# Kernel optimization log

Hardware: AMD Instinct MI355X
Metric: run time of the kernel (lower is better)

The kernel has to match this reference:

```python
import jax, jax.numpy as jnp
import numpy as np

B, S, E, H = 4, 2048, 1024, 64

def setup_inputs() -> dict:
    key = jax.random.key(0)
    k1, k2, k3, k4 = jax.random.split(key, 4)
    return {
        "x": jax.random.normal(k1, (B, S, E), dtype=jnp.float32),
        "Wq": jax.random.normal(k2, (E, H), dtype=jnp.float32) * (E ** -0.5),
        "Wk": jax.random.normal(k3, (E, H), dtype=jnp.float32) * (E ** -0.5),
        "Wv": jax.random.normal(k4, (E, H), dtype=jnp.float32) * (E ** -0.5),
    }

def reference(x, Wq, Wk, Wv):
    b, s, e = x.shape
    q = jnp.einsum('bse,eh->bsh', x, Wq)   # [B,S,H]
    k = jnp.einsum('bse,eh->bsh', x, Wk)
    v = jnp.einsum('bse,eh->bsh', x, Wv)
    # NOTE: source scales by sqrt(embedding_dimension), not sqrt(head_dim)
    scores = jnp.einsum('bqh,bkh->bqk', q, k) / (e ** 0.5)  # [B,S,S]
    causal = jnp.tril(jnp.ones((s, s), dtype=bool))
    scores = jnp.where(causal, scores, -jnp.inf)
    attn = jax.nn.softmax(scores.astype(jnp.float32), axis=-1)
    return jnp.einsum('bqk,bkh->bqh', attn, v)  # [B,S,H]
```

## Files before the change

### kernel.cpp

```cpp
#include <hip/hip_runtime.h>
#include <hip/hip_bf16.h>
#include <math.h>

#define BB 4
#define SS 2048
#define EE 1024
#define HH 64
#define BS (BB*SS)

typedef __attribute__((ext_vector_type(8))) short bf16x8;
typedef __attribute__((ext_vector_type(4))) float f32x4;

static __device__ __forceinline__ unsigned int f2b(float f) {
  __hip_bfloat16 h = __float2bfloat16(f);
  unsigned short u;
  __builtin_memcpy(&u, &h, 2);
  return (unsigned int)u;
}

__global__ __launch_bounds__(256) void wt_prep(const float* __restrict__ Wq,
                                               const float* __restrict__ Wk,
                                               const float* __restrict__ Wv,
                                               unsigned short* __restrict__ wt) {
  __shared__ float tile[64 * 69];
  const int blk = blockIdx.x;
  const int w = blk >> 4;
  const int et = blk & 15;
  const int t = threadIdx.x;
  const float* __restrict__ W = (w == 0) ? Wq : ((w == 1) ? Wk : Wv);

#pragma unroll
  for (int i = 0; i < 4; ++i) {
    const int idx = t + i * 256;
    const int row = idx >> 4;
    const int f4 = idx & 15;
    const float4 v = *(const float4*)(W + ((size_t)(et * 64 + row)) * 64 + f4 * 4);
    tile[row * 69 + f4 * 4 + 0] = v.x;
    tile[row * 69 + f4 * 4 + 1] = v.y;
    tile[row * 69 + f4 * 4 + 2] = v.z;
    tile[row * 69 + f4 * 4 + 3] = v.w;
  }
  __syncthreads();

  const float scale = (w == 0) ? 0.03125f * 1.4426950408889634f : 1.0f;
  const int h = t >> 2;
  const int eg = (t & 3) * 16;
  unsigned int o[8];
#pragma unroll
  for (int i = 0; i < 8; ++i) {
    const float a = tile[(eg + 2 * i + 0) * 69 + h] * scale;
    const float b = tile[(eg + 2 * i + 1) * 69 + h] * scale;
    o[i] = f2b(a) | (f2b(b) << 16);
  }
  unsigned short* dst = wt + ((size_t)(w * 64 + h)) * 1024 + et * 64 + eg;
  uint4 lo4; lo4.x = o[0]; lo4.y = o[1]; lo4.z = o[2]; lo4.w = o[3];
  uint4 hi4; hi4.x = o[4]; hi4.y = o[5]; hi4.z = o[6]; hi4.w = o[7];
  *(uint4*)dst = lo4;
  *(uint4*)(dst + 8) = hi4;
}

__global__ __launch_bounds__(512) void qkv_mfma(const float* __restrict__ x,
                                                const unsigned short* __restrict__ wt,
                                                unsigned short* __restrict__ qb,
                                                unsigned short* __restrict__ kbuf,
                                                unsigned short* __restrict__ vtb) {
  __shared__ char smem[57344];
  const int t = threadIdx.x;
  const int blk = blockIdx.x;
  const int lane = t & 63;
  const int wv = t >> 6;
  const int wm = wv >> 2;
  const int wn = wv & 3;
  const int lo = lane & 15, hi = lane >> 4;

  const int xrow = t >> 4;
  const int xf4 = t & 15;
  const int wr0 = t >> 3;
  const int wc = t & 7;

  const float* __restrict__ xsrc = x + ((size_t)blk * 32 + xrow) * 1024 + xf4 * 4;
  const unsigned short* __restrict__ wsrc = wt + (size_t)wr0 * 1024 + wc * 8;

  float4 xr;
  bf16x8 wrg[3];

  f32x4 acc[3] = {};

#define LOADT(kt)                                                     \
  do {                                                                \
    xr = *(const float4*)(xsrc + (kt) * 64);                          \
    wrg[0] = *(const bf16x8*)(wsrc + (kt) * 64);                      \
    wrg[1] = *(const bf16x8*)(wsrc + 64 * 1024 + (kt) * 64);          \
    wrg[2] = *(const bf16x8*)(wsrc + 128 * 1024 + (kt) * 64);         \
  } while (0)

#define WRITET(buf)                                                          \
  do {                                                                       \
    uint2 pv;                                                                \
    pv.x = f2b(xr.x) | (f2b(xr.y) << 16);                                    \
    pv.y = f2b(xr.z) | (f2b(xr.w) << 16);                                    \
    *(uint2*)&smem[(buf) * 4096 + xrow * 128 +                               \
                   ((xf4 * 8) ^ ((xrow & 7) << 4))] = pv;                    \
    char* wb = &smem[8192 + (buf) * 24576];                                  \
    const int sw = (wc * 16) ^ ((wr0 & 7) << 4);                             \
    *(bf16x8*)&wb[(wr0 + 0) * 128 + sw] = wrg[0];                            \
    *(bf16x8*)&wb[(wr0 + 64) * 128 + sw] = wrg[1];                           \
    *(bf16x8*)&wb[(wr0 + 128) * 128 + sw] = wrg[2];                          \
  } while (0)

  LOADT(0);
  WRITET(0);
  __syncthreads();

  const int arow = wm * 16 + lo;
  const int aswz = (arow & 7) << 4;

  for (int kt = 0; kt < 16; ++kt) {
    const int cur = kt & 1;
    if (kt < 15) LOADT(kt + 1);

    const char* xb = &smem[cur * 4096];
    const char* wb = &smem[8192 + cur * 24576];
    const bf16x8 a0 = *(const bf16x8*)&xb[arow * 128 + ((hi * 16) ^ aswz)];
    const bf16x8 a1 = *(const bf16x8*)&xb[arow * 128 + ((64 + hi * 16) ^ aswz)];
#pragma unroll
    for (int nf = 0; nf < 3; ++nf) {
      const int brow = wn * 48 + nf * 16 + lo;
      const int bswz = (brow & 7) << 4;
      const bf16x8 b0 = *(const bf16x8*)&wb[brow * 128 + ((hi * 16) ^ bswz)];
      const bf16x8 b1 = *(const bf16x8*)&wb[brow * 128 + ((64 + hi * 16) ^ bswz)];
      acc[nf] = __builtin_amdgcn_mfma_f32_16x16x32_bf16(a0, b0, acc[nf], 0, 0, 0);
      acc[nf] = __builtin_amdgcn_mfma_f32_16x16x32_bf16(a1, b1, acc[nf], 0, 0, 0);
    }

    if (kt < 15) WRITET(cur ^ 1);
    __syncthreads();
  }

  const int m0 = blk * 32 + wm * 16 + hi * 4;
#pragma unroll
  for (int nf = 0; nf < 3; ++nf) {
    const int nb = wn * 48 + nf * 16;
    const int which = nb >> 6;
    const int h = (nb & 63) + lo;
#pragma unroll
    for (int r = 0; r < 4; ++r) {
      const int row = m0 + r;
      const unsigned short v = (unsigned short)f2b(acc[nf][r]);
      if (which == 0) qb[(size_t)row * 64 + h] = v;
      else if (which == 1) kbuf[(size_t)row * 64 + h] = v;
      else vtb[((size_t)(row >> 11) * 64 + h) * 2048 + (row & 2047)] = v;
    }
  }
#undef LOADT
#undef WRITET
}

__global__ __launch_bounds__(512) void attn_mfma(const unsigned short* __restrict__ qb,
                                                 const unsigned short* __restrict__ kbuf,
                                                 const unsigned short* __restrict__ vt,
                                                 float* __restrict__ out) {
  __shared__ __align__(16) float sacc[8][16][64];
  __shared__ float sml[2][8][16];

  const int t = threadIdx.x;
  const int lane = t & 63;
  const int w = t >> 6;
  const int lo = lane & 15, hi = lane >> 4;
  const int hi4 = hi * 4;

  const int blk = blockIdx.x;
  const int batch = blk & 3;
  const int tt = blk >> 2;
  const int qt = (tt & 1) ? (63 - (tt >> 1)) : (tt >> 1);
  const int q0 = qt * 32;

  const unsigned short* Qb = qb   + (size_t)batch * SS * 64;
  const unsigned short* Kb = kbuf + (size_t)batch * SS * 64;
  const unsigned short* Vt = vt   + (size_t)batch * 64 * SS;

  const int qA = q0 + lo;
  const int qBr = q0 + 16 + lo;

  const bf16x8 qf0a = *(const bf16x8*)(Qb + (size_t)qA * 64 + hi * 8);
  const bf16x8 qf1a = *(const bf16x8*)(Qb + (size_t)qA * 64 + 32 + hi * 8);
  const bf16x8 qf0b = *(const bf16x8*)(Qb + (size_t)qBr * 64 + hi * 8);
  const bf16x8 qf1b = *(const bf16x8*)(Qb + (size_t)qBr * 64 + 32 + hi * 8);

  f32x4 accA[4] = {}, accB[4] = {};
  float mA = -1e30f, lA = 0.f, mB = -1e30f, lB = 0.f;

  const int kend = q0 + 32;
  for (int kbase = w * 64; kbase < kend; kbase += 512) {
    f32x4 sA[4], sB[4];
    __builtin_amdgcn_s_setprio(1);
#pragma unroll
    for (int j0 = 0; j0 < 4; ++j0) {
      const unsigned short* Krow = Kb + (size_t)(kbase + j0 * 16 + lo) * 64 + hi * 8;
      const bf16x8 ka = *(const bf16x8*)(Krow);
      const bf16x8 kb2 = *(const bf16x8*)(Krow + 32);
      f32x4 ca = {}, cb = {};
      ca = __builtin_amdgcn_mfma_f32_16x16x32_bf16(ka, qf0a, ca, 0, 0, 0);
      ca = __builtin_amdgcn_mfma_f32_16x16x32_bf16(kb2, qf1a, ca, 0, 0, 0);
      cb = __builtin_amdgcn_mfma_f32_16x16x32_bf16(ka, qf0b, cb, 0, 0, 0);
      cb = __builtin_amdgcn_mfma_f32_16x16x32_bf16(kb2, qf1b, cb, 0, 0, 0);
      sA[j0] = ca; sB[j0] = cb;
    }
    __builtin_amdgcn_s_setprio(0);

    bf16x8 va[2][4];
#pragma unroll
    for (int kc = 0; kc < 2; ++kc)
#pragma unroll
      for (int j = 0; j < 4; ++j)
        va[kc][j] = *(const bf16x8*)(Vt + (size_t)(j * 16 + lo) * SS +
                                     kbase + kc * 32 + hi * 8);

    if (kbase + 64 > q0) {
#pragma unroll
      for (int j0 = 0; j0 < 4; ++j0)
#pragma unroll
        for (int r = 0; r < 4; ++r) {
          const int key = kbase + j0 * 16 + hi4 + r;
          sA[j0][r] = (key > qA) ? -1e30f : sA[j0][r];
          sB[j0][r] = (key > qBr) ? -1e30f : sB[j0][r];
        }
    }

    unsigned int WA[4][2], WB[4][2];
    {
      float mx = fmaxf(fmaxf(sA[0][0], sA[0][1]), fmaxf(sA[0][2], sA[0][3]));
      mx = fmaxf(mx, fmaxf(fmaxf(sA[1][0], sA[1][1]), fmaxf(sA[1][2], sA[1][3])));
      mx = fmaxf(mx, fmaxf(fmaxf(sA[2][0], sA[2][1]), fmaxf(sA[2][2], sA[2][3])));
      mx = fmaxf(mx, fmaxf(fmaxf(sA[3][0], sA[3][1]), fmaxf(sA[3][2], sA[3][3])));
      mx = fmaxf(mx, __shfl_xor(mx, 16));
      mx = fmaxf(mx, __shfl_xor(mx, 32));
      if (__any(mx > mA)) {
        const float mnew = fmaxf(mA, mx);
        const float sc = exp2f(mA - mnew);
        mA = mnew;
        lA *= sc;
#pragma unroll
        for (int j = 0; j < 4; ++j) {
          accA[j][0] *= sc; accA[j][1] *= sc;
          accA[j][2] *= sc; accA[j][3] *= sc;
        }
      }
      float ps = 0.f;
#pragma unroll
      for (int j0 = 0; j0 < 4; ++j0) {
        const float p0 = exp2f(sA[j0][0] - mA);
        const float p1 = exp2f(sA[j0][1] - mA);
        const float p2 = exp2f(sA[j0][2] - mA);
        const float p3 = exp2f(sA[j0][3] - mA);
        ps += (p0 + p1) + (p2 + p3);
        WA[j0][0] = f2b(p0) | (f2b(p1) << 16);
        WA[j0][1] = f2b(p2) | (f2b(p3) << 16);
      }
      ps += __shfl_xor(ps, 16);
      ps += __shfl_xor(ps, 32);
      lA += ps;
    }
    {
      float mx = fmaxf(fmaxf(sB[0][0], sB[0][1]), fmaxf(sB[0][2], sB[0][3]));
      mx = fmaxf(mx, fmaxf(fmaxf(sB[1][0], sB[1][1]), fmaxf(sB[1][2], sB[1][3])));
      mx = fmaxf(mx, fmaxf(fmaxf(sB[2][0], sB[2][1]), fmaxf(sB[2][2], sB[2][3])));
      mx = fmaxf(mx, fmaxf(fmaxf(sB[3][0], sB[3][1]), fmaxf(sB[3][2], sB[3][3])));
      mx = fmaxf(mx, __shfl_xor(mx, 16));
      mx = fmaxf(mx, __shfl_xor(mx, 32));
      if (__any(mx > mB)) {
        const float mnew = fmaxf(mB, mx);
        const float sc = exp2f(mB - mnew);
        mB = mnew;
        lB *= sc;
#pragma unroll
        for (int j = 0; j < 4; ++j) {
          accB[j][0] *= sc; accB[j][1] *= sc;
          accB[j][2] *= sc; accB[j][3] *= sc;
        }
      }
      float ps = 0.f;
#pragma unroll
      for (int j0 = 0; j0 < 4; ++j0) {
        const float p0 = exp2f(sB[j0][0] - mB);
        const float p1 = exp2f(sB[j0][1] - mB);
        const float p2 = exp2f(sB[j0][2] - mB);
        const float p3 = exp2f(sB[j0][3] - mB);
        ps += (p0 + p1) + (p2 + p3);
        WB[j0][0] = f2b(p0) | (f2b(p1) << 16);
        WB[j0][1] = f2b(p2) | (f2b(p3) << 16);
      }
      ps += __shfl_xor(ps, 16);
      ps += __shfl_xor(ps, 32);
      lB += ps;
    }

#pragma unroll
    for (int kc = 0; kc < 2; ++kc) {
      unsigned int wra[4], wrb[4];
#pragma unroll
      for (int wi = 0; wi < 4; ++wi) {
        const int src = lo + ((lane & 16) << 1) + ((wi >> 1) << 4);
        const unsigned int a0 = (unsigned int)__shfl((int)WA[2 * kc + 0][wi & 1], src);
        const unsigned int a1 = (unsigned int)__shfl((int)WA[2 * kc + 1][wi & 1], src);
        const unsigned int b0 = (unsigned int)__shfl((int)WB[2 * kc + 0][wi & 1], src);
        const unsigned int b1 = (unsigned int)__shfl((int)WB[2 * kc + 1][wi & 1], src);
        wra[wi] = (hi < 2) ? a0 : a1;
        wrb[wi] = (hi < 2) ? b0 : b1;
      }
      bf16x8 pBA, pBB;
      __builtin_memcpy(&pBA, wra, 16);
      __builtin_memcpy(&pBB, wrb, 16);
      __builtin_amdgcn_s_setprio(1);
#pragma unroll
      for (int j = 0; j < 4; ++j) {
        accA[j] = __builtin_amdgcn_mfma_f32_16x16x32_bf16(va[kc][j], pBA, accA[j], 0, 0, 0);
        accB[j] = __builtin_amdgcn_mfma_f32_16x16x32_bf16(va[kc][j], pBB, accB[j], 0, 0, 0);
      }
      __builtin_amdgcn_s_setprio(0);
    }
  }

  if (hi == 0) { sml[0][w][lo] = mA; sml[1][w][lo] = lA; }
#pragma unroll
  for (int j = 0; j < 4; ++j)
    *(f32x4*)&sacc[w][lo][j * 16 + hi4] = accA[j];
  __syncthreads();
  {
    const int row = t >> 5;
    const int d0 = (t & 31) * 2;
    float mstar = sml[0][0][row];
#pragma unroll
    for (int ww = 1; ww < 8; ++ww) mstar = fmaxf(mstar, sml[0][ww][row]);
    float lstar = 0.f, o0 = 0.f, o1 = 0.f;
#pragma unroll
    for (int ww = 0; ww < 8; ++ww) {
      const float f = exp2f(sml[0][ww][row] - mstar);
      lstar += sml[1][ww][row] * f;
      const float2 a2 = *(const float2*)&sacc[ww][row][d0];
      o0 += a2.x * f;
      o1 += a2.y * f;
    }
    const float rl = 1.0f / lstar;
    float2 o; o.x = o0 * rl; o.y = o1 * rl;
    *(float2*)(out + ((size_t)batch * SS + q0 + row) * 64 + d0) = o;
  }
  __syncthreads();

  if (hi == 0) { sml[0][w][lo] = mB; sml[1][w][lo] = lB; }
#pragma unroll
  for (int j = 0; j < 4; ++j)
    *(f32x4*)&sacc[w][lo][j * 16 + hi4] = accB[j];
  __syncthreads();
  {
    const int row = t >> 5;
    const int d0 = (t & 31) * 2;
    float mstar = sml[0][0][row];
#pragma unroll
    for (int ww = 1; ww < 8; ++ww) mstar = fmaxf(mstar, sml[0][ww][row]);
    float lstar = 0.f, o0 = 0.f, o1 = 0.f;
#pragma unroll
    for (int ww = 0; ww < 8; ++ww) {
      const float f = exp2f(sml[0][ww][row] - mstar);
      lstar += sml[1][ww][row] * f;
      const float2 a2 = *(const float2*)&sacc[ww][row][d0];
      o0 += a2.x * f;
      o1 += a2.y * f;
    }
    const float rl = 1.0f / lstar;
    float2 o; o.x = o0 * rl; o.y = o1 * rl;
    *(float2*)(out + ((size_t)batch * SS + q0 + 16 + row) * 64 + d0) = o;
  }
}

extern "C" void kernel_launch(void* const* d_in, const int* in_sizes, int n_in,
                              void* d_out, int out_size, void* d_ws, size_t ws_size,
                              hipStream_t stream) {
  const float* x  = (const float*)d_in[0];
  const float* Wq = (const float*)d_in[1];
  const float* Wk = (const float*)d_in[2];
  const float* Wv = (const float*)d_in[3];
  float* outp = (float*)d_out;

  unsigned short* qb = (unsigned short*)d_ws;
  unsigned short* kb = qb + (size_t)BS * 64;
  unsigned short* vt = kb + (size_t)BS * 64;
  unsigned short* wt = vt + (size_t)BS * 64;

  wt_prep<<<48, 256, 0, stream>>>(Wq, Wk, Wv, wt);
  qkv_mfma<<<BS / 32, 512, 0, stream>>>(x, wt, qb, kb, vt);
  attn_mfma<<<256, 512, 0, stream>>>(qb, kb, vt, outp);
}
```

Baseline: 46.82 us.

## Load weights via global_load_lds and prefetch K fragments one chunk ahead

In the QKV projection kernel, the pre-swizzled bf16 weight tiles now go straight from global memory into LDS with global_load_lds instead of passing through registers, which removes VGPR staging and the LDS store instructions. The global addresses are computed with the inverse swizzle so the LDS layout stays the same. In the attention kernel, the K fragments for the next 512-key chunk are loaded into a second register set while the current chunk is processed, hiding global load latency at the cost of more registers and possible lower occupancy.

```diff
diff --git a/kernel.cpp b/kernel.cpp
--- a/kernel.cpp
+++ b/kernel.cpp
@@ -75,41 +75,53 @@
 
   const int xrow = t >> 4;
   const int xf4 = t & 15;
-  const int wr0 = t >> 3;
-  const int wc = t & 7;
 
   const float* __restrict__ xsrc = x + ((size_t)blk * 32 + xrow) * 1024 + xf4 * 4;
-  const unsigned short* __restrict__ wsrc = wt + (size_t)wr0 * 1024 + wc * 8;
+
+  const int oW0 = t * 16;
+  const int oW1 = t * 16 + 8192;
+  const int oW2 = t * 16 + 16384;
+  const int n0 = oW0 >> 7, n1 = oW1 >> 7, n2 = oW2 >> 7;
+  const unsigned short* __restrict__ wg0 =
+      wt + (size_t)n0 * 1024 + (((oW0 & 127) ^ ((n0 & 7) << 4)) >> 1);
+  const unsigned short* __restrict__ wg1 =
+      wt + (size_t)n1 * 1024 + (((oW1 & 127) ^ ((n1 & 7) << 4)) >> 1);
+  const unsigned short* __restrict__ wg2 =
+      wt + (size_t)n2 * 1024 + (((oW2 & 127) ^ ((n2 & 7) << 4)) >> 1);
 
   float4 xr;
-  bf16x8 wrg[3];
-
   f32x4 acc[3] = {};
 
-#define LOADT(kt)                                                     \
-  do {                                                                \
-    xr = *(const float4*)(xsrc + (kt) * 64);                          \
-    wrg[0] = *(const bf16x8*)(wsrc + (kt) * 64);                      \
-    wrg[1] = *(const bf16x8*)(wsrc + 64 * 1024 + (kt) * 64);          \
-    wrg[2] = *(const bf16x8*)(wsrc + 128 * 1024 + (kt) * 64);         \
+#define GLOADW(buf, kt)                                                       \
+  do {                                                                        \
+    __builtin_amdgcn_global_load_lds(                                         \
+        (const __attribute__((address_space(1))) void*)(wg0 + (kt) * 64),     \
+        (__attribute__((address_space(3))) void*)&smem[8192 + (buf) * 24576 + oW0], \
+        16, 0, 0);                                                            \
+    __builtin_amdgcn_global_load_lds(                                         \
+        (const __attribute__((address_space(1))) void*)(wg1 + (kt) * 64),     \
+        (__attribute__((address_space(3))) void*)&smem[8192 + (buf) * 24576 + oW1], \
+        16, 0, 0);                                                            \
+    __builtin_amdgcn_global_load_lds(                                         \
+        (const __attribute__((address_space(1))) void*)(wg2 + (kt) * 64),     \
+        (__attribute__((address_space(3))) void*)&smem[8192 + (buf) * 24576 + oW2], \
+        16, 0, 0);                                                            \
   } while (0)
 
-#define WRITET(buf)                                                          \
+#define LOADX(kt) xr = *(const float4*)(xsrc + (kt) * 64)
+
+#define WRITEX(buf)                                                          \
   do {                                                                       \
     uint2 pv;                                                                \
     pv.x = f2b(xr.x) | (f2b(xr.y) << 16);                                    \
     pv.y = f2b(xr.z) | (f2b(xr.w) << 16);                                    \
     *(uint2*)&smem[(buf) * 4096 + xrow * 128 +                               \
                    ((xf4 * 8) ^ ((xrow & 7) << 4))] = pv;                    \
-    char* wb = &smem[8192 + (buf) * 24576];                                  \
-    const int sw = (wc * 16) ^ ((wr0 & 7) << 4);                             \
-    *(bf16x8*)&wb[(wr0 + 0) * 128 + sw] = wrg[0];                            \
-    *(bf16x8*)&wb[(wr0 + 64) * 128 + sw] = wrg[1];                           \
-    *(bf16x8*)&wb[(wr0 + 128) * 128 + sw] = wrg[2];                          \
   } while (0)
 
-  LOADT(0);
-  WRITET(0);
+  GLOADW(0, 0);
+  LOADX(0);
+  WRITEX(0);
   __syncthreads();
 
   const int arow = wm * 16 + lo;
@@ -117,7 +129,10 @@
 
   for (int kt = 0; kt < 16; ++kt) {
     const int cur = kt & 1;
-    if (kt < 15) LOADT(kt + 1);
+    if (kt < 15) {
+      LOADX(kt + 1);
+      GLOADW(cur ^ 1, kt + 1);
+    }
 
     const char* xb = &smem[cur * 4096];
     const char* wb = &smem[8192 + cur * 24576];
@@ -133,7 +148,7 @@
       acc[nf] = __builtin_amdgcn_mfma_f32_16x16x32_bf16(a1, b1, acc[nf], 0, 0, 0);
     }
 
-    if (kt < 15) WRITET(cur ^ 1);
+    if (kt < 15) WRITEX(cur ^ 1);
     __syncthreads();
   }
 
@@ -152,8 +167,9 @@
       else vtb[((size_t)(row >> 11) * 64 + h) * 2048 + (row & 2047)] = v;
     }
   }
-#undef LOADT
-#undef WRITET
+#undef GLOADW
+#undef LOADX
+#undef WRITEX
 }
 
 __global__ __launch_bounds__(512) void attn_mfma(const unsigned short* __restrict__ qb,
@@ -191,19 +207,26 @@
   float mA = -1e30f, lA = 0.f, mB = -1e30f, lB = 0.f;
 
   const int kend = q0 + 32;
-  for (int kbase = w * 64; kbase < kend; kbase += 512) {
+
+  auto loadk = [&](bf16x8 (&dst)[8], int kb) {
+#pragma unroll
+    for (int j0 = 0; j0 < 4; ++j0) {
+      const unsigned short* Krow = Kb + (size_t)(kb + j0 * 16 + lo) * 64 + hi * 8;
+      dst[2 * j0 + 0] = *(const bf16x8*)(Krow);
+      dst[2 * j0 + 1] = *(const bf16x8*)(Krow + 32);
+    }
+  };
+
+  auto process_chunk = [&](int kb, const bf16x8 (&kf)[8]) {
     f32x4 sA[4], sB[4];
     __builtin_amdgcn_s_setprio(1);
 #pragma unroll
     for (int j0 = 0; j0 < 4; ++j0) {
-      const unsigned short* Krow = Kb + (size_t)(kbase + j0 * 16 + lo) * 64 + hi * 8;
-      const bf16x8 ka = *(const bf16x8*)(Krow);
-      const bf16x8 kb2 = *(const bf16x8*)(Krow + 32);
       f32x4 ca = {}, cb = {};
-      ca = __builtin_amdgcn_mfma_f32_16x16x32_bf16(ka, qf0a, ca, 0, 0, 0);
-      ca = __builtin_amdgcn_mfma_f32_16x16x32_bf16(kb2, qf1a, ca, 0, 0, 0);
-      cb = __builtin_amdgcn_mfma_f32_16x16x32_bf16(ka, qf0b, cb, 0, 0, 0);
-      cb = __builtin_amdgcn_mfma_f32_16x16x32_bf16(kb2, qf1b, cb, 0, 0, 0);
+      ca = __builtin_amdgcn_mfma_f32_16x16x32_bf16(kf[2 * j0], qf0a, ca, 0, 0, 0);
+      ca = __builtin_amdgcn_mfma_f32_16x16x32_bf16(kf[2 * j0 + 1], qf1a, ca, 0, 0, 0);
+      cb = __builtin_amdgcn_mfma_f32_16x16x32_bf16(kf[2 * j0], qf0b, cb, 0, 0, 0);
+      cb = __builtin_amdgcn_mfma_f32_16x16x32_bf16(kf[2 * j0 + 1], qf1b, cb, 0, 0, 0);
       sA[j0] = ca; sB[j0] = cb;
     }
     __builtin_amdgcn_s_setprio(0);
@@ -214,14 +237,14 @@
 #pragma unroll
       for (int j = 0; j < 4; ++j)
         va[kc][j] = *(const bf16x8*)(Vt + (size_t)(j * 16 + lo) * SS +
-                                     kbase + kc * 32 + hi * 8);
-
-    if (kbase + 64 > q0) {
+                                     kb + kc * 32 + hi * 8);
+
+    if (kb + 64 > q0) {
 #pragma unroll
       for (int j0 = 0; j0 < 4; ++j0)
 #pragma unroll
         for (int r = 0; r < 4; ++r) {
-          const int key = kbase + j0 * 16 + hi4 + r;
+          const int key = kb + j0 * 16 + hi4 + r;
           sA[j0][r] = (key > qA) ? -1e30f : sA[j0][r];
           sB[j0][r] = (key > qBr) ? -1e30f : sB[j0][r];
         }
@@ -319,6 +342,25 @@
       }
       __builtin_amdgcn_s_setprio(0);
     }
+  };
+
+  {
+    bf16x8 kfA[8], kfB[8];
+    int kbase = w * 64;
+    bool useA = true;
+    if (kbase < kend) loadk(kfA, kbase);
+    while (kbase < kend) {
+      const int kn = kbase + 512;
+      if (useA) {
+        if (kn < kend) loadk(kfB, kn);
+        process_chunk(kbase, kfA);
+      } else {
+        if (kn < kend) loadk(kfA, kn);
+        process_chunk(kbase, kfB);
+      }
+      useA = !useA;
+      kbase = kn;
+    }
   }
 
   if (hi == 0) { sml[0][w][lo] = mA; sml[1][w][lo] = lA; }
```

After: 52.23 us. 11.5% more time.

## Fuse weight prep, QKV projection and attention into one persistent kernel with grid barriers

Applied to the files above, without the earlier changes.

Merges the three launches into a single 256-block kernel. The stages are separated by a hierarchical atomic grid barrier (8-way, then 8-way, then 4-way counters plus a release flag), and the barrier memory is cleared with a memset before each launch. The aim is to remove kernel launch gaps and tail effects between stages. The risks are spin-wait overhead, the assumption that all 256 blocks of 512 threads and 57 KB of LDS are co-resident, and an extra memset launch.

```diff
diff --git a/kernel.cpp b/kernel.cpp
--- a/kernel.cpp
+++ b/kernel.cpp
@@ -18,358 +18,374 @@
   return (unsigned int)u;
 }
 
-__global__ __launch_bounds__(256) void wt_prep(const float* __restrict__ Wq,
-                                               const float* __restrict__ Wk,
-                                               const float* __restrict__ Wv,
-                                               unsigned short* __restrict__ wt) {
-  __shared__ float tile[64 * 69];
-  const int blk = blockIdx.x;
-  const int w = blk >> 4;
-  const int et = blk & 15;
-  const int t = threadIdx.x;
-  const float* __restrict__ W = (w == 0) ? Wq : ((w == 1) ? Wk : Wv);
-
-#pragma unroll
-  for (int i = 0; i < 4; ++i) {
-    const int idx = t + i * 256;
-    const int row = idx >> 4;
-    const int f4 = idx & 15;
-    const float4 v = *(const float4*)(W + ((size_t)(et * 64 + row)) * 64 + f4 * 4);
-    tile[row * 69 + f4 * 4 + 0] = v.x;
-    tile[row * 69 + f4 * 4 + 1] = v.y;
-    tile[row * 69 + f4 * 4 + 2] = v.z;
-    tile[row * 69 + f4 * 4 + 3] = v.w;
+static __device__ __forceinline__ void grid_bar(unsigned* __restrict__ B, int round) {
+  __syncthreads();
+  if (threadIdx.x == 0) {
+    __builtin_amdgcn_fence(__ATOMIC_RELEASE, "agent");
+    const int g0 = blockIdx.x >> 3;
+    unsigned v = __hip_atomic_fetch_add(B + g0 * 32, 1u,
+                    __ATOMIC_RELAXED, __HIP_MEMORY_SCOPE_AGENT);
+    if (v == (unsigned)(round * 8 + 7)) {
+      const int g1 = g0 >> 3;
+      unsigned v1 = __hip_atomic_fetch_add(B + (32 + g1) * 32, 1u,
+                       __ATOMIC_RELAXED, __HIP_MEMORY_SCOPE_AGENT);
+      if (v1 == (unsigned)(round * 8 + 7)) {
+        unsigned vr = __hip_atomic_fetch_add(B + 36 * 32, 1u,
+                         __ATOMIC_RELAXED, __HIP_MEMORY_SCOPE_AGENT);
+        if (vr == (unsigned)(round * 4 + 3))
+          __hip_atomic_store(B + 37 * 32, (unsigned)(round + 1),
+                             __ATOMIC_RELEASE, __HIP_MEMORY_SCOPE_AGENT);
+      }
+    }
+    while (__hip_atomic_load(B + 37 * 32, __ATOMIC_RELAXED,
+                             __HIP_MEMORY_SCOPE_AGENT) <= (unsigned)round)
+      __builtin_amdgcn_s_sleep(16);
+    __builtin_amdgcn_fence(__ATOMIC_ACQUIRE, "agent");
   }
   __syncthreads();
-
-  const float scale = (w == 0) ? 0.03125f * 1.4426950408889634f : 1.0f;
-  const int h = t >> 2;
-  const int eg = (t & 3) * 16;
-  unsigned int o[8];
-#pragma unroll
-  for (int i = 0; i < 8; ++i) {
-    const float a = tile[(eg + 2 * i + 0) * 69 + h] * scale;
-    const float b = tile[(eg + 2 * i + 1) * 69 + h] * scale;
-    o[i] = f2b(a) | (f2b(b) << 16);
-  }
-  unsigned short* dst = wt + ((size_t)(w * 64 + h)) * 1024 + et * 64 + eg;
-  uint4 lo4; lo4.x = o[0]; lo4.y = o[1]; lo4.z = o[2]; lo4.w = o[3];
-  uint4 hi4; hi4.x = o[4]; hi4.y = o[5]; hi4.z = o[6]; hi4.w = o[7];
-  *(uint4*)dst = lo4;
-  *(uint4*)(dst + 8) = hi4;
 }
 
-__global__ __launch_bounds__(512) void qkv_mfma(const float* __restrict__ x,
-                                                const unsigned short* __restrict__ wt,
-                                                unsigned short* __restrict__ qb,
-                                                unsigned short* __restrict__ kbuf,
-                                                unsigned short* __restrict__ vtb) {
-  __shared__ char smem[57344];
+__global__ __launch_bounds__(512) void fused_all(
+    const float* __restrict__ x, const float* __restrict__ Wq,
+    const float* __restrict__ Wk, const float* __restrict__ Wv,
+    unsigned short* __restrict__ wt, unsigned short* __restrict__ qb,
+    unsigned short* __restrict__ kbuf, unsigned short* __restrict__ vtb,
+    float* __restrict__ out, unsigned* __restrict__ bar) {
+  __shared__ __align__(16) char smem[57344];
+
   const int t = threadIdx.x;
   const int blk = blockIdx.x;
   const int lane = t & 63;
-  const int wv = t >> 6;
-  const int wm = wv >> 2;
-  const int wn = wv & 3;
   const int lo = lane & 15, hi = lane >> 4;
 
-  const int xrow = t >> 4;
-  const int xf4 = t & 15;
-  const int wr0 = t >> 3;
-  const int wc = t & 7;
-
-  const float* __restrict__ xsrc = x + ((size_t)blk * 32 + xrow) * 1024 + xf4 * 4;
-  const unsigned short* __restrict__ wsrc = wt + (size_t)wr0 * 1024 + wc * 8;
-
-  float4 xr;
-  bf16x8 wrg[3];
-
-  f32x4 acc[3] = {};
+  if (blk < 48) {
+    float* tile = (float*)smem;
+    const int w = blk >> 4;
+    const int et = blk & 15;
+    const float* __restrict__ W = (w == 0) ? Wq : ((w == 1) ? Wk : Wv);
+#pragma unroll
+    for (int i = 0; i < 2; ++i) {
+      const int idx = t + i * 512;
+      const int row = idx >> 4;
+      const int f4 = idx & 15;
+      const float4 v = *(const float4*)(W + ((size_t)(et * 64 + row)) * 64 + f4 * 4);
+      tile[row * 69 + f4 * 4 + 0] = v.x;
+      tile[row * 69 + f4 * 4 + 1] = v.y;
+      tile[row * 69 + f4 * 4 + 2] = v.z;
+      tile[row * 69 + f4 * 4 + 3] = v.w;
+    }
+    __syncthreads();
+    const float scale = (w == 0) ? 0.03125f * 1.4426950408889634f : 1.0f;
+    const int h = t >> 3;
+    const int eg = (t & 7) * 8;
+    unsigned int o[4];
+#pragma unroll
+    for (int i = 0; i < 4; ++i) {
+      const float a = tile[(eg + 2 * i + 0) * 69 + h] * scale;
+      const float b = tile[(eg + 2 * i + 1) * 69 + h] * scale;
+      o[i] = f2b(a) | (f2b(b) << 16);
+    }
+    uint4 pk; pk.x = o[0]; pk.y = o[1]; pk.z = o[2]; pk.w = o[3];
+    *(uint4*)(wt + ((size_t)(w * 64 + h)) * 1024 + et * 64 + eg) = pk;
+  }
+  grid_bar(bar, 0);
+
+  {
+    const int wv = t >> 6;
+    const int wm = wv >> 2;
+    const int wn = wv & 3;
+
+    const int xrow = t >> 4;
+    const int xf4 = t & 15;
+    const int wr0 = t >> 3;
+    const int wc = t & 7;
+
+    const float* __restrict__ xsrc = x + ((size_t)blk * 32 + xrow) * 1024 + xf4 * 4;
+    const unsigned short* __restrict__ wsrc = wt + (size_t)wr0 * 1024 + wc * 8;
+
+    float4 xr;
+    bf16x8 wrg[3];
+    f32x4 acc[3] = {};
 
 #define LOADT(kt)                                                     \
-  do {                                                                \
-    xr = *(const float4*)(xsrc + (kt) * 64);                          \
-    wrg[0] = *(const bf16x8*)(wsrc + (kt) * 64);                      \
-    wrg[1] = *(const bf16x8*)(wsrc + 64 * 1024 + (kt) * 64);          \
-    wrg[2] = *(const bf16x8*)(wsrc + 128 * 1024 + (kt) * 64);         \
-  } while (0)
+    do {                                                              \
+      xr = *(const float4*)(xsrc + (kt) * 64);                        \
+      wrg[0] = *(const bf16x8*)(wsrc + (kt) * 64);                    \
+      wrg[1] = *(const bf16x8*)(wsrc + 64 * 1024 + (kt) * 64);        \
+      wrg[2] = *(const bf16x8*)(wsrc + 128 * 1024 + (kt) * 64);       \
+    } while (0)
 
 #define WRITET(buf)                                                          \
-  do {                                                                       \
-    uint2 pv;                                                                \
-    pv.x = f2b(xr.x) | (f2b(xr.y) << 16);                                    \
-    pv.y = f2b(xr.z) | (f2b(xr.w) << 16);                                    \
-    *(uint2*)&smem[(buf) * 4096 + xrow * 128 +                               \
-                   ((xf4 * 8) ^ ((xrow & 7) << 4))] = pv;                    \
-    char* wb = &smem[8192 + (buf) * 24576];                                  \
-    const int sw = (wc * 16) ^ ((wr0 & 7) << 4);                             \
-    *(bf16x8*)&wb[(wr0 + 0) * 128 + sw] = wrg[0];                            \
-    *(bf16x8*)&wb[(wr0 + 64) * 128 + sw] = wrg[1];                           \
-    *(bf16x8*)&wb[(wr0 + 128) * 128 + sw] = wrg[2];                          \
-  } while (0)
-
-  LOADT(0);
-  WRITET(0);
-  __syncthreads();
-
-  const int arow = wm * 16 + lo;
-  const int aswz = (arow & 7) << 4;
-
-  for (int kt = 0; kt < 16; ++kt) {
-    const int cur = kt & 1;
-    if (kt < 15) LOADT(kt + 1);
-
-    const char* xb = &smem[cur * 4096];
-    const char* wb = &smem[8192 + cur * 24576];
-    const bf16x8 a0 = *(const bf16x8*)&xb[arow * 128 + ((hi * 16) ^ aswz)];
-    const bf16x8 a1 = *(const bf16x8*)&xb[arow * 128 + ((64 + hi * 16) ^ aswz)];
+    do {                                                                     \
+      uint2 pv;                                                              \
+      pv.x = f2b(xr.x) | (f2b(xr.y) << 16);                                  \
+      pv.y = f2b(xr.z) | (f2b(xr.w) << 16);                                  \
+      *(uint2*)&smem[(buf) * 4096 + xrow * 128 +                             \
+                     ((xf4 * 8) ^ ((xrow & 7) << 4))] = pv;                  \
+      char* wb = &smem[8192 + (buf) * 24576];                                \
+      const int sw = (wc * 16) ^ ((wr0 & 7) << 4);                           \
+      *(bf16x8*)&wb[(wr0 + 0) * 128 + sw] = wrg[0];                          \
+      *(bf16x8*)&wb[(wr0 + 64) * 128 + sw] = wrg[1];                         \
+      *(bf16x8*)&wb[(wr0 + 128) * 128 + sw] = wrg[2];                        \
+    } while (0)
+
+    LOADT(0);
+    WRITET(0);
+    __syncthreads();
+
+    const int arow = wm * 16 + lo;
+    const int aswz = (arow & 7) << 4;
+
+    for (int kt = 0; kt < 16; ++kt) {
+      const int cur = kt & 1;
+      if (kt < 15) LOADT(kt + 1);
+
+      const char* xb = &smem[cur * 4096];
+      const char* wb = &smem[8192 + cur * 24576];
+      const bf16x8 a0 = *(const bf16x8*)&xb[arow * 128 + ((hi * 16) ^ aswz)];
+      const bf16x8 a1 = *(const bf16x8*)&xb[arow * 128 + ((64 + hi * 16) ^ aswz)];
+#pragma unroll
+      for (int nf = 0; nf < 3; ++nf) {
+        const int brow = wn * 48 + nf * 16 + lo;
+        const int bswz = (brow & 7) << 4;
+        const bf16x8 b0 = *(const bf16x8*)&wb[brow * 128 + ((hi * 16) ^ bswz)];
+        const bf16x8 b1 = *(const bf16x8*)&wb[brow * 128 + ((64 + hi * 16) ^ bswz)];
+        acc[nf] = __builtin_amdgcn_mfma_f32_16x16x32_bf16(a0, b0, acc[nf], 0, 0, 0);
+        acc[nf] = __builtin_amdgcn_mfma_f32_16x16x32_bf16(a1, b1, acc[nf], 0, 0, 0);
+      }
+
+      if (kt < 15) WRITET(cur ^ 1);
+      __syncthreads();
+    }
+
+    const int m0 = blk * 32 + wm * 16 + hi * 4;
 #pragma unroll
     for (int nf = 0; nf < 3; ++nf) {
-      const int brow = wn * 48 + nf * 16 + lo;
-      const int bswz = (brow & 7) << 4;
-      const bf16x8 b0 = *(const bf16x8*)&wb[brow * 128 + ((hi * 16) ^ bswz)];
-      const bf16x8 b1 = *(const bf16x8*)&wb[brow * 128 + ((64 + hi * 16) ^ bswz)];
-      acc[nf] = __builtin_amdgcn_mfma_f32_16x16x32_bf16(a0, b0, acc[nf], 0, 0, 0);
-      acc[nf] = __builtin_amdgcn_mfma_f32_16x16x32_bf16(a1, b1, acc[nf], 0, 0, 0);
-    }
-
-    if (kt < 15) WRITET(cur ^ 1);
-    __syncthreads();
-  }
-
-  const int m0 = blk * 32 + wm * 16 + hi * 4;
-#pragma unroll
-  for (int nf = 0; nf < 3; ++nf) {
-    const int nb = wn * 48 + nf * 16;
-    const int which = nb >> 6;
-    const int h = (nb & 63) + lo;
-#pragma unroll
-    for (int r = 0; r < 4; ++r) {
-      const int row = m0 + r;
-      const unsigned short v = (unsigned short)f2b(acc[nf][r]);
-      if (which == 0) qb[(size_t)row * 64 + h] = v;
-      else if (which == 1) kbuf[(size_t)row * 64 + h] = v;
-      else vtb[((size_t)(row >> 11) * 64 + h) * 2048 + (row & 2047)] = v;
-    }
-  }
+      const int nb = wn * 48 + nf * 16;
+      const int which = nb >> 6;
+      const int h = (nb & 63) + lo;
+#pragma unroll
+      for (int r = 0; r < 4; ++r) {
+        const int row = m0 + r;
+        const unsigned short v = (unsigned short)f2b(acc[nf][r]);
+        if (which == 0) qb[(size_t)row * 64 + h] = v;
+        else if (which == 1) kbuf[(size_t)row * 64 + h] = v;
+        else vtb[((size_t)(row >> 11) * 64 + h) * 2048 + (row & 2047)] = v;
+      }
+    }
 #undef LOADT
 #undef WRITET
-}
-
-__global__ __launch_bounds__(512) void attn_mfma(const unsigned short* __restrict__ qb,
-                                                 const unsigned short* __restrict__ kbuf,
-                                                 const unsigned short* __restrict__ vt,
-                                                 float* __restrict__ out) {
-  __shared__ __align__(16) float sacc[8][16][64];
-  __shared__ float sml[2][8][16];
-
-  const int t = threadIdx.x;
-  const int lane = t & 63;
-  const int w = t >> 6;
-  const int lo = lane & 15, hi = lane >> 4;
-  const int hi4 = hi * 4;
-
-  const int blk = blockIdx.x;
-  const int batch = blk & 3;
-  const int tt = blk >> 2;
-  const int qt = (tt & 1) ? (63 - (tt >> 1)) : (tt >> 1);
-  const int q0 = qt * 32;
-
-  const unsigned short* Qb = qb   + (size_t)batch * SS * 64;
-  const unsigned short* Kb = kbuf + (size_t)batch * SS * 64;
-  const unsigned short* Vt = vt   + (size_t)batch * 64 * SS;
-
-  const int qA = q0 + lo;
-  const int qBr = q0 + 16 + lo;
-
-  const bf16x8 qf0a = *(const bf16x8*)(Qb + (size_t)qA * 64 + hi * 8);
-  const bf16x8 qf1a = *(const bf16x8*)(Qb + (size_t)qA * 64 + 32 + hi * 8);
-  const bf16x8 qf0b = *(const bf16x8*)(Qb + (size_t)qBr * 64 + hi * 8);
-  const bf16x8 qf1b = *(const bf16x8*)(Qb + (size_t)qBr * 64 + 32 + hi * 8);
-
-  f32x4 accA[4] = {}, accB[4] = {};
-  float mA = -1e30f, lA = 0.f, mB = -1e30f, lB = 0.f;
-
-  const int kend = q0 + 32;
-  for (int kbase = w * 64; kbase < kend; kbase += 512) {
-    f32x4 sA[4], sB[4];
-    __builtin_amdgcn_s_setprio(1);
-#pragma unroll
-    for (int j0 = 0; j0 < 4; ++j0) {
-      const unsigned short* Krow = Kb + (size_t)(kbase + j0 * 16 + lo) * 64 + hi * 8;
-      const bf16x8 ka = *(const bf16x8*)(Krow);
-      const bf16x8 kb2 = *(const bf16x8*)(Krow + 32);
-      f32x4 ca = {}, cb = {};
-      ca = __builtin_amdgcn_mfma_f32_16x16x32_bf16(ka, qf0a, ca, 0, 0, 0);
-      ca = __builtin_amdgcn_mfma_f32_16x16x32_bf16(kb2, qf1a, ca, 0, 0, 0);
-      cb = __builtin_amdgcn_mfma_f32_16x16x32_bf16(ka, qf0b, cb, 0, 0, 0);
-      cb = __builtin_amdgcn_mfma_f32_16x16x32_bf16(kb2, qf1b, cb, 0, 0, 0);
-      sA[j0] = ca; sB[j0] = cb;
-    }
-    __builtin_amdgcn_s_setprio(0);
-
-    bf16x8 va[2][4];
-#pragma unroll
-    for (int kc = 0; kc < 2; ++kc)
-#pragma unroll
-      for (int j = 0; j < 4; ++j)
-        va[kc][j] = *(const bf16x8*)(Vt + (size_t)(j * 16 + lo) * SS +
-                                     kbase + kc * 32 + hi * 8);
-
-    if (kbase + 64 > q0) {
-#pragma unroll
-      for (int j0 = 0; j0 < 4; ++j0)
-#pragma unroll
-        for (int r = 0; r < 4; ++r) {
-          const int key = kbase + j0 * 16 + hi4 + r;
-          sA[j0][r] = (key > qA) ? -1e30f : sA[j0][r];
-          sB[j0][r] = (key > qBr) ? -1e30f : sB[j0][r];
-        }
-    }
-
-    unsigned int WA[4][2], WB[4][2];
+  }
+  grid_bar(bar, 1);
+
+  {
+    float (*sacc)[16][64] = (float(*)[16][64])smem;
+    float (*sml)[8][16]   = (float(*)[8][16])(smem + 32768);
+
+    const int w = t >> 6;
+    const int hi4 = hi * 4;
+
+    const int batch = blk & 3;
+    const int tt = blk >> 2;
+    const int qt = (tt & 1) ? (63 - (tt >> 1)) : (tt >> 1);
+    const int q0 = qt * 32;
+
+    const unsigned short* Qb = qb   + (size_t)batch * SS * 64;
+    const unsigned short* Kb = kbuf + (size_t)batch * SS * 64;
+    const unsigned short* Vt = vtb  + (size_t)batch * 64 * SS;
+
+    const int qA = q0 + lo;
+    const int qBr = q0 + 16 + lo;
+
+    const bf16x8 qf0a = *(const bf16x8*)(Qb + (size_t)qA * 64 + hi * 8);
+    const bf16x8 qf1a = *(const bf16x8*)(Qb + (size_t)qA * 64 + 32 + hi * 8);
+    const bf16x8 qf0b = *(const bf16x8*)(Qb + (size_t)qBr * 64 + hi * 8);
+    const bf16x8 qf1b = *(const bf16x8*)(Qb + (size_t)qBr * 64 + 32 + hi * 8);
+
+    f32x4 accA[4] = {}, accB[4] = {};
+    float mA = -1e30f, lA = 0.f, mB = -1e30f, lB = 0.f;
+
+    const int kend = q0 + 32;
+    for (int kbase = w * 64; kbase < kend; kbase += 512) {
+      f32x4 sA[4], sB[4];
+      __builtin_amdgcn_s_setprio(1);
+#pragma unroll
+      for (int j0 = 0; j0 < 4; ++j0) {
+        const unsigned short* Krow = Kb + (size_t)(kbase + j0 * 16 + lo) * 64 + hi * 8;
+        const bf16x8 ka = *(const bf16x8*)(Krow);
+        const bf16x8 kb2 = *(const bf16x8*)(Krow + 32);
+        f32x4 ca = {}, cb = {};
+        ca = __builtin_amdgcn_mfma_f32_16x16x32_bf16(ka, qf0a, ca, 0, 0, 0);
+        ca = __builtin_amdgcn_mfma_f32_16x16x32_bf16(kb2, qf1a, ca, 0, 0, 0);
+        cb = __builtin_amdgcn_mfma_f32_16x16x32_bf16(ka, qf0b, cb, 0, 0, 0);
+        cb = __builtin_amdgcn_mfma_f32_16x16x32_bf16(kb2, qf1b, cb, 0, 0, 0);
+        sA[j0] = ca; sB[j0] = cb;
+      }
+      __builtin_amdgcn_s_setprio(0);
+
+      bf16x8 va[2][4];
+#pragma unroll
+      for (int kc = 0; kc < 2; ++kc)
+#pragma unroll
+        for (int j = 0; j < 4; ++j)
+          va[kc][j] = *(const bf16x8*)(Vt + (size_t)(j * 16 + lo) * SS +
+                                       kbase + kc * 32 + hi * 8);
+
+      if (kbase + 64 > q0) {
+#pragma unroll
+        for (int j0 = 0; j0 < 4; ++j0)
+#pragma unroll
+          for (int r = 0; r < 4; ++r) {
+            const int key = kbase + j0 * 16 + hi4 + r;
+            sA[j0][r] = (key > qA) ? -1e30f : sA[j0][r];
+            sB[j0][r] = (key > qBr) ? -1e30f : sB[j0][r];
+          }
+      }
+
+      unsigned int WA[4][2], WB[4][2];
+      {
+        float mx = fmaxf(fmaxf(sA[0][0], sA[0][1]), fmaxf(sA[0][2], sA[0][3]));
+        mx = fmaxf(mx, fmaxf(fmaxf(sA[1][0], sA[1][1]), fmaxf(sA[1][2], sA[1][3])));
+        mx = fmaxf(mx, fmaxf(fmaxf(sA[2][0], sA[2][1]), fmaxf(sA[2][2], sA[2][3])));
+        mx = fmaxf(mx, fmaxf(fmaxf(sA[3][0], sA[3][1]), fmaxf(sA[3][2], sA[3][3])));
+        mx = fmaxf(mx, __shfl_xor(mx, 16));
+        mx = fmaxf(mx, __shfl_xor(mx, 32));
+        if (__any(mx > mA)) {
+          const float mnew = fmaxf(mA, mx);
+          const float sc = exp2f(mA - mnew);
+          mA = mnew;
+          lA *= sc;
+#pragma unroll
+          for (int j = 0; j < 4; ++j) {
+            accA[j][0] *= sc; accA[j][1] *= sc;
+            accA[j][2] *= sc; accA[j][3] *= sc;
+          }
+        }
+        float ps = 0.f;
+#pragma unroll
+        for (int j0 = 0; j0 < 4; ++j0) {
+          const float p0 = exp2f(sA[j0][0] - mA);
+          const float p1 = exp2f(sA[j0][1] - mA);
+          const float p2 = exp2f(sA[j0][2] - mA);
+          const float p3 = exp2f(sA[j0][3] - mA);
+          ps += (p0 + p1) + (p2 + p3);
+          WA[j0][0] = f2b(p0) | (f2b(p1) << 16);
+          WA[j0][1] = f2b(p2) | (f2b(p3) << 16);
+        }
+        ps += __shfl_xor(ps, 16);
+        ps += __shfl_xor(ps, 32);
+        lA += ps;
+      }
+      {
+        float mx = fmaxf(fmaxf(sB[0][0], sB[0][1]), fmaxf(sB[0][2], sB[0][3]));
+        mx = fmaxf(mx, fmaxf(fmaxf(sB[1][0], sB[1][1]), fmaxf(sB[1][2], sB[1][3])));
+        mx = fmaxf(mx, fmaxf(fmaxf(sB[2][0], sB[2][1]), fmaxf(sB[2][2], sB[2][3])));
+        mx = fmaxf(mx, fmaxf(fmaxf(sB[3][0], sB[3][1]), fmaxf(sB[3][2], sB[3][3])));
+        mx = fmaxf(mx, __shfl_xor(mx, 16));
+        mx = fmaxf(mx, __shfl_xor(mx, 32));
+        if (__any(mx > mB)) {
+          const float mnew = fmaxf(mB, mx);
+          const float sc = exp2f(mB - mnew);
+          mB = mnew;
+          lB *= sc;
+#pragma unroll
+          for (int j = 0; j < 4; ++j) {
+            accB[j][0] *= sc; accB[j][1] *= sc;
+            accB[j][2] *= sc; accB[j][3] *= sc;
+          }
+        }
+        float ps = 0.f;
+#pragma unroll
+        for (int j0 = 0; j0 < 4; ++j0) {
+          const float p0 = exp2f(sB[j0][0] - mB);
+          const float p1 = exp2f(sB[j0][1] - mB);
+          const float p2 = exp2f(sB[j0][2] - mB);
+          const float p3 = exp2f(sB[j0][3] - mB);
+          ps += (p0 + p1) + (p2 + p3);
+          WB[j0][0] = f2b(p0) | (f2b(p1) << 16);
+          WB[j0][1] = f2b(p2) | (f2b(p3) << 16);
+        }
+        ps += __shfl_xor(ps, 16);
+        ps += __shfl_xor(ps, 32);
+        lB += ps;
+      }
+
+#pragma unroll
+      for (int kc = 0; kc < 2; ++kc) {
+        unsigned int wra[4], wrb[4];
+#pragma unroll
+        for (int wi = 0; wi < 4; ++wi) {
+          const int src = lo + ((lane & 16) << 1) + ((wi >> 1) << 4);
+          const unsigned int a0 = (unsigned int)__shfl((int)WA[2 * kc + 0][wi & 1], src);
+          const unsigned int a1 = (unsigned int)__shfl((int)WA[2 * kc + 1][wi & 1], src);
+          const unsigned int b0 = (unsigned int)__shfl((int)WB[2 * kc + 0][wi & 1], src);
+          const unsigned int b1 = (unsigned int)__shfl((int)WB[2 * kc + 1][wi & 1], src);
+          wra[wi] = (hi < 2) ? a0 : a1;
+          wrb[wi] = (hi < 2) ? b0 : b1;
+        }
+        bf16x8 pBA, pBB;
+        __builtin_memcpy(&pBA, wra, 16);
+        __builtin_memcpy(&pBB, wrb, 16);
+        __builtin_amdgcn_s_setprio(1);
+#pragma unroll
+        for (int j = 0; j < 4; ++j) {
+          accA[j] = __builtin_amdgcn_mfma_f32_16x16x32_bf16(va[kc][j], pBA, accA[j], 0, 0, 0);
+          accB[j] = __builtin_amdgcn_mfma_f32_16x16x32_bf16(va[kc][j], pBB, accB[j], 0, 0, 0);
+        }
+        __builtin_amdgcn_s_setprio(0);
+      }
+    }
+
+    if (hi == 0) { sml[0][w][lo] = mA; sml[1][w][lo] = lA; }
+#pragma unroll
+    for (int j = 0; j < 4; ++j)
+      *(f32x4*)&sacc[w][lo][j * 16 + hi4] = accA[j];
+    __syncthreads();
     {
-      float mx = fmaxf(fmaxf(sA[0][0], sA[0][1]), fmaxf(sA[0][2], sA[0][3]));
-      mx = fmaxf(mx, fmaxf(fmaxf(sA[1][0], sA[1][1]), fmaxf(sA[1][2], sA[1][3])));
-      mx = fmaxf(mx, fmaxf(fmaxf(sA[2][0], sA[2][1]), fmaxf(sA[2][2], sA[2][3])));
-      mx = fmaxf(mx, fmaxf(fmaxf(sA[3][0], sA[3][1]), fmaxf(sA[3][2], sA[3][3])));
-      mx = fmaxf(mx, __shfl_xor(mx, 16));
-      mx = fmaxf(mx, __shfl_xor(mx, 32));
-      if (__any(mx > mA)) {
-        const float mnew = fmaxf(mA, mx);
-        const float sc = exp2f(mA - mnew);
-        mA = mnew;
-        lA *= sc;
-#pragma unroll
-        for (int j = 0; j < 4; ++j) {
-          accA[j][0] *= sc; accA[j][1] *= sc;
-          accA[j][2] *= sc; accA[j][3] *= sc;
-        }
-      }
-      float ps = 0.f;
-#pragma unroll
-      for (int j0 = 0; j0 < 4; ++j0) {
-        const float p0 = exp2f(sA[j0][0] - mA);
-        const float p1 = exp2f(sA[j0][1] - mA);
-        const float p2 = exp2f(sA[j0][2] - mA);
-        const float p3 = exp2f(sA[j0][3] - mA);
-        ps += (p0 + p1) + (p2 + p3);
-        WA[j0][0] = f2b(p0) | (f2b(p1) << 16);
-        WA[j0][1] = f2b(p2) | (f2b(p3) << 16);
-      }
-      ps += __shfl_xor(ps, 16);
-      ps += __shfl_xor(ps, 32);
-      lA += ps;
-    }
+      const int row = t >> 5;
+      const int d0 = (t & 31) * 2;
+      float mstar = sml[0][0][row];
+#pragma unroll
+      for (int ww = 1; ww < 8; ++ww) mstar = fmaxf(mstar, sml[0][ww][row]);
+      float lstar = 0.f, o0 = 0.f, o1 = 0.f;
+#pragma unroll
+      for (int ww = 0; ww < 8; ++ww) {
+        const float f = exp2f(sml[0][ww][row] - mstar);
+        lstar += sml[1][ww][row] * f;
+        const float2 a2 = *(const float2*)&sacc[ww][row][d0];
+        o0 += a2.x * f;
+        o1 += a2.y * f;
+      }
+      const float rl = 1.0f / lstar;
+      float2 o; o.x = o0 * rl; o.y = o1 * rl;
+      *(float2*)(out + ((size_t)batch * SS + q0 + row) * 64 + d0) = o;
+    }
+    __syncthreads();
+
+    if (hi == 0) { sml[0][w][lo] = mB; sml[1][w][lo] = lB; }
+#pragma unroll
+    for (int j = 0; j < 4; ++j)
+      *(f32x4*)&sacc[w][lo][j * 16 + hi4] = accB[j];
+    __syncthreads();
     {
-      float mx = fmaxf(fmaxf(sB[0][0], sB[0][1]), fmaxf(sB[0][2], sB[0][3]));
-      mx = fmaxf(mx, fmaxf(fmaxf(sB[1][0], sB[1][1]), fmaxf(sB[1][2], sB[1][3])));
-      mx = fmaxf(mx, fmaxf(fmaxf(sB[2][0], sB[2][1]), fmaxf(sB[2][2], sB[2][3])));
-      mx = fmaxf(mx, fmaxf(fmaxf(sB[3][0], sB[3][1]), fmaxf(sB[3][2], sB[3][3])));
-      mx = fmaxf(mx, __shfl_xor(mx, 16));
-      mx = fmaxf(mx, __shfl_xor(mx, 32));
-      if (__any(mx > mB)) {
-        const float mnew = fmaxf(mB, mx);
-        const float sc = exp2f(mB - mnew);
-        mB = mnew;
-        lB *= sc;
-#pragma unroll
-        for (int j = 0; j < 4; ++j) {
-          accB[j][0] *= sc; accB[j][1] *= sc;
-          accB[j][2] *= sc; accB[j][3] *= sc;
-        }
-      }
-      float ps = 0.f;
-#pragma unroll
-      for (int j0 = 0; j0 < 4; ++j0) {
-        const float p0 = exp2f(sB[j0][0] - mB);
-        const float p1 = exp2f(sB[j0][1] - mB);
-        const float p2 = exp2f(sB[j0][2] - mB);
-        const float p3 = exp2f(sB[j0][3] - mB);
-        ps += (p0 + p1) + (p2 + p3);
-        WB[j0][0] = f2b(p0) | (f2b(p1) << 16);
-        WB[j0][1] = f2b(p2) | (f2b(p3) << 16);
-      }
-      ps += __shfl_xor(ps, 16);
-      ps += __shfl_xor(ps, 32);
-      lB += ps;
-    }
-
-#pragma unroll
-    for (int kc = 0; kc < 2; ++kc) {
-      unsigned int wra[4], wrb[4];
-#pragma unroll
-      for (int wi = 0; wi < 4; ++wi) {
-        const int src = lo + ((lane & 16) << 1) + ((wi >> 1) << 4);
-        const unsigned int a0 = (unsigned int)__shfl((int)WA[2 * kc + 0][wi & 1], src);
-        const unsigned int a1 = (unsigned int)__shfl((int)WA[2 * kc + 1][wi & 1], src);
-        const unsigned int b0 = (unsigned int)__shfl((int)WB[2 * kc + 0][wi & 1], src);
-        const unsigned int b1 = (unsigned int)__shfl((int)WB[2 * kc + 1][wi & 1], src);
-        wra[wi] = (hi < 2) ? a0 : a1;
-        wrb[wi] = (hi < 2) ? b0 : b1;
-      }
-      bf16x8 pBA, pBB;
-      __builtin_memcpy(&pBA, wra, 16);
-      __builtin_memcpy(&pBB, wrb, 16);
-      __builtin_amdgcn_s_setprio(1);
-#pragma unroll
-      for (int j = 0; j < 4; ++j) {
-        accA[j] = __builtin_amdgcn_mfma_f32_16x16x32_bf16(va[kc][j], pBA, accA[j], 0, 0, 0);
-        accB[j] = __builtin_amdgcn_mfma_f32_16x16x32_bf16(va[kc][j], pBB, accB[j], 0, 0, 0);
-      }
-      __builtin_amdgcn_s_setprio(0);
-    }
-  }
-
-  if (hi == 0) { sml[0][w][lo] = mA; sml[1][w][lo] = lA; }
-#pragma unroll
-  for (int j = 0; j < 4; ++j)
-    *(f32x4*)&sacc[w][lo][j * 16 + hi4] = accA[j];
-  __syncthreads();
-  {
-    const int row = t >> 5;
-    const int d0 = (t & 31) * 2;
-    float mstar = sml[0][0][row];
-#pragma unroll
-    for (int ww = 1; ww < 8; ++ww) mstar = fmaxf(mstar, sml[0][ww][row]);
-    float lstar = 0.f, o0 = 0.f, o1 = 0.f;
-#pragma unroll
-    for (int ww = 0; ww < 8; ++ww) {
-      const float f = exp2f(sml[0][ww][row] - mstar);
-      lstar += sml[1][ww][row] * f;
-      const float2 a2 = *(const float2*)&sacc[ww][row][d0];
-      o0 += a2.x * f;
-      o1 += a2.y * f;
-    }
-    const float rl = 1.0f / lstar;
-    float2 o; o.x = o0 * rl; o.y = o1 * rl;
-    *(float2*)(out + ((size_t)batch * SS + q0 + row) * 64 + d0) = o;
-  }
-  __syncthreads();
-
-  if (hi == 0) { sml[0][w][lo] = mB; sml[1][w][lo] = lB; }
-#pragma unroll
-  for (int j = 0; j < 4; ++j)
-    *(f32x4*)&sacc[w][lo][j * 16 + hi4] = accB[j];
-  __syncthreads();
-  {
-    const int row = t >> 5;
-    const int d0 = (t & 31) * 2;
-    float mstar = sml[0][0][row];
-#pragma unroll
-    for (int ww = 1; ww < 8; ++ww) mstar = fmaxf(mstar, sml[0][ww][row]);
-    float lstar = 0.f, o0 = 0.f, o1 = 0.f;
-#pragma unroll
-    for (int ww = 0; ww < 8; ++ww) {
-      const float f = exp2f(sml[0][ww][row] - mstar);
-      lstar += sml[1][ww][row] * f;
-      const float2 a2 = *(const float2*)&sacc[ww][row][d0];
-      o0 += a2.x * f;
-      o1 += a2.y * f;
-    }
-    const float rl = 1.0f / lstar;
-    float2 o; o.x = o0 * rl; o.y = o1 * rl;
-    *(float2*)(out + ((size_t)batch * SS + q0 + 16 + row) * 64 + d0) = o;
+      const int row = t >> 5;
+      const int d0 = (t & 31) * 2;
+      float mstar = sml[0][0][row];
+#pragma unroll
+      for (int ww = 1; ww < 8; ++ww) mstar = fmaxf(mstar, sml[0][ww][row]);
+      float lstar = 0.f, o0 = 0.f, o1 = 0.f;
+#pragma unroll
+      for (int ww = 0; ww < 8; ++ww) {
+        const float f = exp2f(sml[0][ww][row] - mstar);
+        lstar += sml[1][ww][row] * f;
+        const float2 a2 = *(const float2*)&sacc[ww][row][d0];
+        o0 += a2.x * f;
+        o1 += a2.y * f;
+      }
+      const float rl = 1.0f / lstar;
+      float2 o; o.x = o0 * rl; o.y = o1 * rl;
+      *(float2*)(out + ((size_t)batch * SS + q0 + 16 + row) * 64 + d0) = o;
+    }
   }
 }
 
@@ -386,8 +402,8 @@
   unsigned short* kb = qb + (size_t)BS * 64;
   unsigned short* vt = kb + (size_t)BS * 64;
   unsigned short* wt = vt + (size_t)BS * 64;
-
-  wt_prep<<<48, 256, 0, stream>>>(Wq, Wk, Wv, wt);
-  qkv_mfma<<<BS / 32, 512, 0, stream>>>(x, wt, qb, kb, vt);
-  attn_mfma<<<256, 512, 0, stream>>>(qb, kb, vt, outp);
+  unsigned* bar = (unsigned*)((char*)d_ws + (4 << 20));
+
+  hipMemsetAsync(bar, 0, 8192, stream);
+  fused_all<<<256, 512, 0, stream>>>(x, Wq, Wk, Wv, wt, qb, kb, vt, outp, bar);
 }
```

Result: slower. 60.44 us (+29.1%).
